# Kernel optimization log

Hardware: AMD Instinct MI355X
Metric: run time of the kernel (lower is better)

The kernel has to match this reference:

```python
import jax, jax.numpy as jnp
import numpy as np

B, C, H, W = 16, 512, 64, 64
R = 8
CP = C // R  # inner channel dim C' = 64


def setup_inputs() -> dict:
    key = jax.random.key(0)
    ks = jax.random.split(key, 10)
    s_in = 1.0 / np.sqrt(C)
    s_cp = 1.0 / np.sqrt(CP)
    return {
        "x": jax.random.normal(ks[0], (B, C, H, W), dtype=jnp.float32),
        "wq": jax.random.uniform(ks[1], (CP, C), jnp.float32, -s_in, s_in),
        "bq": jax.random.uniform(ks[2], (CP,), jnp.float32, -s_in, s_in),
        "wk": jax.random.uniform(ks[3], (CP, C), jnp.float32, -s_in, s_in),
        "bk": jax.random.uniform(ks[4], (CP,), jnp.float32, -s_in, s_in),
        "wv": jax.random.uniform(ks[5], (CP, C), jnp.float32, -s_in, s_in),
        "bv": jax.random.uniform(ks[6], (CP,), jnp.float32, -s_in, s_in),
        "wo": jax.random.uniform(ks[7], (C, CP), jnp.float32, -s_cp, s_cp),
        "bo": jax.random.uniform(ks[8], (C,), jnp.float32, -s_cp, s_cp),
        # torch init is gamma=0 (output==x, zero grads to convs); use small
        # nonzero value so the reference exercises the full graph.
        "gamma": jax.random.normal(ks[9], (1,), dtype=jnp.float32) * 0.1,
    }


def reference(x, wq, bq, wk, bk, wv, bv, wo, bo, gamma):
    b, c, h, w = x.shape
    n = h * w
    xf = x.reshape(b, c, n)  # flatten spatial -> (B, C, N)
    # 1x1 convs == channel matmuls
    q = jnp.einsum("oc,bcn->bon", wq, xf) + bq[:, None]  # (B, C', N)
    k = jnp.einsum("oc,bcn->bon", wk, xf) + bk[:, None]  # (B, C', N)
    v = jnp.einsum("oc,bcn->bon", wv, xf) + bv[:, None]  # (B, C', N)
    # energy = bmm(key (B,C',N), query^T (B,N,C')) -> (B, C', C')
    energy = jnp.einsum("bin,bjn->bij", k, q)
    attention = jax.nn.softmax(energy, axis=-1)  # (B, C', C')
    out = jnp.einsum("bij,bjn->bin", attention, v)  # (B, C', N)
    out = jnp.einsum("co,bon->bcn", wo, out) + bo[:, None]  # (B, C, N)
    out = out.reshape(b, c, h, w)
    return gamma * out + x
```

## Files before the change

kernel.cpp:

```cpp
#include <hip/hip_runtime.h>
#include <hip/hip_bf16.h>


#define NN 4096
#define CIN 512
#define CPD 64

typedef short s8v __attribute__((ext_vector_type(8)));
typedef float f4v __attribute__((ext_vector_type(4)));

__device__ __forceinline__ unsigned short f2bf(float f) {
    union { float f; unsigned int u; } c; c.f = f;
    unsigned int r = c.u + 0x7FFFu + ((c.u >> 16) & 1u);
    return (unsigned short)(r >> 16);
}

__global__ __launch_bounds__(256) void k_prep(
    const float* __restrict__ x, unsigned short* __restrict__ xt, int b_base)
{
    const int nt = blockIdx.x;
    const int ct = blockIdx.y;
    const int bl = blockIdx.z;
    const int b  = b_base + bl;
    __shared__ unsigned short lds[64][68];
    const int t = threadIdx.x;

    const float* xb = x + ((size_t)b * CIN + ct * 64) * NN + nt * 64;
    #pragma unroll
    for (int i = 0; i < 4; ++i) {
        int c = i * 16 + (t >> 4);
        int n = (t & 15) * 4;
        float4 v = *(const float4*)(xb + (size_t)c * NN + n);
        lds[c][n]     = f2bf(v.x);
        lds[c][n + 1] = f2bf(v.y);
        lds[c][n + 2] = f2bf(v.z);
        lds[c][n + 3] = f2bf(v.w);
    }
    __syncthreads();
    unsigned short* xtb = xt + ((size_t)bl * NN + nt * 64) * CIN + ct * 64;
    #pragma unroll
    for (int pass = 0; pass < 2; ++pass) {
        int n  = (t >> 3) + pass * 32;
        int c8 = (t & 7) * 8;
        unsigned short tmp[8];
        #pragma unroll
        for (int j = 0; j < 8; ++j) tmp[j] = lds[c8 + j][n];
        *(uint4*)(xtb + (size_t)n * CIN + c8) = *(const uint4*)tmp;
    }
}

__global__ __launch_bounds__(256) void k_qkv(
    const unsigned short* __restrict__ xt,
    const float* __restrict__ wq, const float* __restrict__ bq,
    const float* __restrict__ wk, const float* __restrict__ bk,
    const float* __restrict__ wv, const float* __restrict__ bv,
    unsigned short* __restrict__ q, unsigned short* __restrict__ k,
    unsigned short* __restrict__ vt, int b_base)
{
    const int nb = blockIdx.x;
    const int p  = blockIdx.y;
    const int bl = blockIdx.z;
    const int b  = b_base + bl;
    const float* w    = (p == 0) ? wq : (p == 1) ? wk : wv;
    const float* bias = (p == 0) ? bq : (p == 1) ? bk : bv;

    __shared__ unsigned short wl[64 * 512];
    const int t = threadIdx.x;

    #pragma unroll
    for (int i = 0; i < 16; ++i) {
        int lin = i * 256 + t;
        int o   = lin >> 6;
        int c8  = (lin & 63) * 8;
        float4 v0 = *(const float4*)(w + (size_t)o * CIN + c8);
        float4 v1 = *(const float4*)(w + (size_t)o * CIN + c8 + 4);
        unsigned short tmp[8] = { f2bf(v0.x), f2bf(v0.y), f2bf(v0.z), f2bf(v0.w),
                                  f2bf(v1.x), f2bf(v1.y), f2bf(v1.z), f2bf(v1.w) };
        int sw = c8 ^ ((o & 7) * 8);
        *(uint4*)(wl + o * 512 + sw) = *(const uint4*)tmp;
    }
    __syncthreads();

    const int wv_  = t >> 6;
    const int L    = t & 63;
    const int quad = L >> 4;
    const int l15  = L & 15;
    const int n0   = nb * 256 + wv_ * 64;
    const unsigned short* xb = xt + (size_t)bl * NN * CIN;

    f4v acc[4][4];
    #pragma unroll
    for (int a = 0; a < 4; ++a)
        #pragma unroll
        for (int d = 0; d < 4; ++d) acc[a][d] = (f4v){0.f, 0.f, 0.f, 0.f};

    #pragma unroll
    for (int ks = 0; ks < 16; ++ks) {
        const int c = ks * 32 + quad * 8;
        s8v bfr[4];
        #pragma unroll
        for (int nt2 = 0; nt2 < 4; ++nt2)
            bfr[nt2] = *(const s8v*)(xb + (size_t)(n0 + nt2 * 16 + l15) * CIN + c);
        s8v afr[4];
        #pragma unroll
        for (int ot = 0; ot < 4; ++ot) {
            int o = ot * 16 + l15;
            afr[ot] = *(const s8v*)(wl + o * 512 + (c ^ ((o & 7) * 8)));
        }
        #pragma unroll
        for (int ot = 0; ot < 4; ++ot)
            #pragma unroll
            for (int nt2 = 0; nt2 < 4; ++nt2)
                acc[ot][nt2] = __builtin_amdgcn_mfma_f32_16x16x32_bf16(
                    afr[ot], bfr[nt2], acc[ot][nt2], 0, 0, 0);
    }

    if (p < 2) {
        unsigned short* outp = ((p == 0) ? q : k) + (size_t)b * CPD * NN;
        #pragma unroll
        for (int ot = 0; ot < 4; ++ot)
            #pragma unroll
            for (int r = 0; r < 4; ++r) {
                int o = ot * 16 + quad * 4 + r;
                float bs = bias[o];
                #pragma unroll
                for (int nt2 = 0; nt2 < 4; ++nt2) {
                    int n = n0 + nt2 * 16 + l15;
                    outp[(size_t)o * NN + n] = f2bf(acc[ot][nt2][r] + bs);
                }
            }
    } else {
        unsigned short* outp = vt + (size_t)b * NN * CPD;
        #pragma unroll
        for (int nt2 = 0; nt2 < 4; ++nt2) {
            int n = n0 + nt2 * 16 + l15;
            #pragma unroll
            for (int ot = 0; ot < 4; ++ot) {
                unsigned short tmp[4];
                #pragma unroll
                for (int r = 0; r < 4; ++r) {
                    int o = ot * 16 + quad * 4 + r;
                    tmp[r] = f2bf(acc[ot][nt2][r] + bias[o]);
                }
                *(uint2*)(outp + (size_t)n * CPD + ot * 16 + quad * 4) = *(const uint2*)tmp;
            }
        }
    }
}

__global__ __launch_bounds__(64) void k_energy(
    const unsigned short* __restrict__ q, const unsigned short* __restrict__ k,
    float* __restrict__ epart)
{
    const int s = blockIdx.x;
    const int b = blockIdx.y;
    const int L = threadIdx.x;
    const int quad = L >> 4, l15 = L & 15;
    const unsigned short* kb = k + (size_t)b * CPD * NN;
    const unsigned short* qb = q + (size_t)b * CPD * NN;

    f4v acc[4][4];
    #pragma unroll
    for (int a = 0; a < 4; ++a)
        #pragma unroll
        for (int d = 0; d < 4; ++d) acc[a][d] = (f4v){0.f, 0.f, 0.f, 0.f};

    #pragma unroll
    for (int ks = 0; ks < 2; ++ks) {
        const int n = s * 64 + ks * 32 + quad * 8;
        s8v af[4], bf_[4];
        #pragma unroll
        for (int it = 0; it < 4; ++it)
            af[it] = *(const s8v*)(kb + (size_t)(it * 16 + l15) * NN + n);
        #pragma unroll
        for (int jt = 0; jt < 4; ++jt)
            bf_[jt] = *(const s8v*)(qb + (size_t)(jt * 16 + l15) * NN + n);
        #pragma unroll
        for (int it = 0; it < 4; ++it)
            #pragma unroll
            for (int jt = 0; jt < 4; ++jt)
                acc[it][jt] = __builtin_amdgcn_mfma_f32_16x16x32_bf16(
                    af[it], bf_[jt], acc[it][jt], 0, 0, 0);
    }
    float* ep = epart + ((size_t)b * 64 + s) * 4096;
    #pragma unroll
    for (int it = 0; it < 4; ++it)
        #pragma unroll
        for (int jt = 0; jt < 4; ++jt)
            #pragma unroll
            for (int r = 0; r < 4; ++r)
                ep[(it * 16 + quad * 4 + r) * 64 + jt * 16 + l15] = acc[it][jt][r];
}

__global__ __launch_bounds__(64) void k_softmax(
    const float* __restrict__ epart, unsigned short* __restrict__ attn)
{
    const int i = blockIdx.x;
    const int b = blockIdx.y;
    const int j = threadIdx.x;
    const float* ep = epart + (size_t)b * 64 * 4096 + i * 64 + j;
    float s = 0.f;
    #pragma unroll
    for (int sp = 0; sp < 64; ++sp) s += ep[(size_t)sp * 4096];
    float m = s;
    #pragma unroll
    for (int off = 32; off; off >>= 1) m = fmaxf(m, __shfl_xor(m, off));
    float e = __expf(s - m);
    float tot = e;
    #pragma unroll
    for (int off = 32; off; off >>= 1) tot += __shfl_xor(tot, off);
    attn[(size_t)b * 4096 + i * 64 + j] = f2bf(e / tot);
}

__global__ __launch_bounds__(256) void k_attnv(
    const unsigned short* __restrict__ vt, const unsigned short* __restrict__ attn,
    unsigned short* __restrict__ avt)
{
    const int nb = blockIdx.x;
    const int b  = blockIdx.y;
    const int t  = threadIdx.x;
    const int wv_ = t >> 6, L = t & 63, quad = L >> 4, l15 = L & 15;
    const int n0 = nb * 256 + wv_ * 64;
    const unsigned short* vtb = vt + (size_t)b * NN * CPD;
    const unsigned short* ab  = attn + (size_t)b * 4096;

    f4v acc[4][4];
    #pragma unroll
    for (int a = 0; a < 4; ++a)
        #pragma unroll
        for (int d = 0; d < 4; ++d) acc[a][d] = (f4v){0.f, 0.f, 0.f, 0.f};

    #pragma unroll
    for (int ks = 0; ks < 2; ++ks) {
        const int jc = ks * 32 + quad * 8;
        s8v af[4], bf_[4];
        #pragma unroll
        for (int mt = 0; mt < 4; ++mt)
            af[mt] = *(const s8v*)(vtb + (size_t)(n0 + mt * 16 + l15) * CPD + jc);
        #pragma unroll
        for (int it = 0; it < 4; ++it)
            bf_[it] = *(const s8v*)(ab + (size_t)(it * 16 + l15) * 64 + jc);
        #pragma unroll
        for (int mt = 0; mt < 4; ++mt)
            #pragma unroll
            for (int it = 0; it < 4; ++it)
                acc[mt][it] = __builtin_amdgcn_mfma_f32_16x16x32_bf16(
                    af[mt], bf_[it], acc[mt][it], 0, 0, 0);
    }
    unsigned short* ob = avt + (size_t)b * NN * CPD;
    #pragma unroll
    for (int mt = 0; mt < 4; ++mt)
        #pragma unroll
        for (int it = 0; it < 4; ++it) {
            int i = it * 16 + l15;
            #pragma unroll
            for (int r = 0; r < 4; ++r) {
                int n = n0 + mt * 16 + quad * 4 + r;
                ob[(size_t)n * CPD + i] = f2bf(acc[mt][it][r]);
            }
        }
}

__global__ __launch_bounds__(256) void k_out(
    const unsigned short* __restrict__ avt, const float* __restrict__ wo,
    const float* __restrict__ bo, const float* __restrict__ gamma,
    const float* __restrict__ x, float* __restrict__ out)
{
    const int nb = blockIdx.x;
    const int cb = blockIdx.y;
    const int b  = blockIdx.z;
    const int c0 = cb * 64;
    __shared__ unsigned short wl[64][72];
    const int t = threadIdx.x;

    #pragma unroll
    for (int i4 = 0; i4 < 4; ++i4) {
        int row = i4 * 16 + (t >> 4);
        int col = (t & 15) * 4;
        float4 v = *(const float4*)(wo + (size_t)(c0 + row) * CPD + col);
        unsigned short tmp[4] = { f2bf(v.x), f2bf(v.y), f2bf(v.z), f2bf(v.w) };
        *(uint2*)&wl[row][col] = *(const uint2*)tmp;
    }
    __syncthreads();

    const int wv_ = t >> 6, L = t & 63, quad = L >> 4, l15 = L & 15;
    const int n0 = nb * 256 + wv_ * 64;
    const unsigned short* avb = avt + (size_t)b * NN * CPD;

    f4v acc[4][4];
    #pragma unroll
    for (int a = 0; a < 4; ++a)
        #pragma unroll
        for (int d = 0; d < 4; ++d) acc[a][d] = (f4v){0.f, 0.f, 0.f, 0.f};

    #pragma unroll
    for (int ks = 0; ks < 2; ++ks) {
        const int ic = ks * 32 + quad * 8;
        s8v af[4], bf_[4];
        #pragma unroll
        for (int ct = 0; ct < 4; ++ct)
            af[ct] = *(const s8v*)(&wl[ct * 16 + l15][ic]);
        #pragma unroll
        for (int nt = 0; nt < 4; ++nt)
            bf_[nt] = *(const s8v*)(avb + (size_t)(n0 + nt * 16 + l15) * CPD + ic);
        #pragma unroll
        for (int ct = 0; ct < 4; ++ct)
            #pragma unroll
            for (int nt = 0; nt < 4; ++nt)
                acc[ct][nt] = __builtin_amdgcn_mfma_f32_16x16x32_bf16(
                    af[ct], bf_[nt], acc[ct][nt], 0, 0, 0);
    }

    const float g = gamma[0];
    #pragma unroll
    for (int ct = 0; ct < 4; ++ct)
        #pragma unroll
        for (int r = 0; r < 4; ++r) {
            int c = c0 + ct * 16 + quad * 4 + r;
            float bs = bo[c];
            #pragma unroll
            for (int nt = 0; nt < 4; ++nt) {
                int n = n0 + nt * 16 + l15;
                size_t idx = ((size_t)b * CIN + c) * NN + n;
                out[idx] = g * (acc[ct][nt][r] + bs) + x[idx];
            }
        }
}

extern "C" void kernel_launch(void* const* d_in, const int* in_sizes, int n_in,
                              void* d_out, int out_size, void* d_ws, size_t ws_size,
                              hipStream_t stream) {
    const float* x  = (const float*)d_in[0];
    const float* wq = (const float*)d_in[1];
    const float* bq = (const float*)d_in[2];
    const float* wk = (const float*)d_in[3];
    const float* bk = (const float*)d_in[4];
    const float* wv = (const float*)d_in[5];
    const float* bv = (const float*)d_in[6];
    const float* wo = (const float*)d_in[7];
    const float* bo = (const float*)d_in[8];
    const float* gm = (const float*)d_in[9];
    float* out = (float*)d_out;

    char* wsb = (char*)d_ws;
    unsigned short* xt = (unsigned short*)wsb;
    unsigned short* q  = (unsigned short*)(wsb + 33554432);
    unsigned short* k  = (unsigned short*)(wsb + 41943040);
    unsigned short* vt = (unsigned short*)(wsb + 50331648);
    float*          epart = (float*)wsb;
    unsigned short* attn  = (unsigned short*)(wsb + 16777216);
    unsigned short* avt   = (unsigned short*)(wsb + 25165824);

    for (int chunk = 0; chunk < 2; ++chunk) {
        int b_base = chunk * 8;
        k_prep<<<dim3(64, 8, 8), 256, 0, stream>>>(x, xt, b_base);
        k_qkv<<<dim3(16, 3, 8), 256, 0, stream>>>(xt, wq, bq, wk, bk, wv, bv,
                                                  q, k, vt, b_base);
    }
    k_energy<<<dim3(64, 16), 64, 0, stream>>>(q, k, epart);
    k_softmax<<<dim3(64, 16), 64, 0, stream>>>(epart, attn);
    k_attnv<<<dim3(16, 16), 256, 0, stream>>>(vt, attn, avt);
    k_out<<<dim3(16, 8, 16), 256, 0, stream>>>(avt, wo, bo, gm, x, out);
}
```

Measured before the change: 368.9 us.

## Fuse transpose into QKV projection, reduce energy in LDS, fuse attn-V with output conv

Removes the separate x transpose/bf16 prep kernel. The QKV kernel now reads fp32 x directly, converts it in registers, and computes all three projections per block, so x is read once instead of three times. The energy kernel uses 4 waves with an LDS atomic reduction, producing 8 partials instead of 64, which shrinks the softmax reduction. The attention-V product and output 1x1 conv are fused so the intermediate stays in LDS, at the cost of uncoalesced column-wise fp32 loads of x and a 64KB LDS weight tile per block.

```diff
diff --git a/kernel.cpp b/kernel.cpp
--- a/kernel.cpp
+++ b/kernel.cpp
@@ -15,159 +15,148 @@
     return (unsigned short)(r >> 16);
 }
 
-__global__ __launch_bounds__(256) void k_prep(
-    const float* __restrict__ x, unsigned short* __restrict__ xt, int b_base)
-{
-    const int nt = blockIdx.x;
-    const int ct = blockIdx.y;
-    const int bl = blockIdx.z;
-    const int b  = b_base + bl;
-    __shared__ unsigned short lds[64][68];
-    const int t = threadIdx.x;
-
-    const float* xb = x + ((size_t)b * CIN + ct * 64) * NN + nt * 64;
-    #pragma unroll
-    for (int i = 0; i < 4; ++i) {
-        int c = i * 16 + (t >> 4);
-        int n = (t & 15) * 4;
-        float4 v = *(const float4*)(xb + (size_t)c * NN + n);
-        lds[c][n]     = f2bf(v.x);
-        lds[c][n + 1] = f2bf(v.y);
-        lds[c][n + 2] = f2bf(v.z);
-        lds[c][n + 3] = f2bf(v.w);
-    }
-    __syncthreads();
-    unsigned short* xtb = xt + ((size_t)bl * NN + nt * 64) * CIN + ct * 64;
-    #pragma unroll
-    for (int pass = 0; pass < 2; ++pass) {
-        int n  = (t >> 3) + pass * 32;
-        int c8 = (t & 7) * 8;
-        unsigned short tmp[8];
-        #pragma unroll
-        for (int j = 0; j < 8; ++j) tmp[j] = lds[c8 + j][n];
-        *(uint4*)(xtb + (size_t)n * CIN + c8) = *(const uint4*)tmp;
-    }
-}
-
-__global__ __launch_bounds__(256) void k_qkv(
-    const unsigned short* __restrict__ xt,
+__global__ __launch_bounds__(512, 2) void k_qkv(
+    const float* __restrict__ x,
     const float* __restrict__ wq, const float* __restrict__ bq,
     const float* __restrict__ wk, const float* __restrict__ bk,
     const float* __restrict__ wv, const float* __restrict__ bv,
     unsigned short* __restrict__ q, unsigned short* __restrict__ k,
-    unsigned short* __restrict__ vt, int b_base)
+    unsigned short* __restrict__ vt)
 {
-    const int nb = blockIdx.x;
-    const int p  = blockIdx.y;
-    const int bl = blockIdx.z;
-    const int b  = b_base + bl;
-    const float* w    = (p == 0) ? wq : (p == 1) ? wk : wv;
-    const float* bias = (p == 0) ? bq : (p == 1) ? bk : bv;
-
-    __shared__ unsigned short wl[64 * 512];
+    const int nb = blockIdx.x, b = blockIdx.y;
     const int t = threadIdx.x;
-
-    #pragma unroll
-    for (int i = 0; i < 16; ++i) {
-        int lin = i * 256 + t;
-        int o   = lin >> 6;
-        int c8  = (lin & 63) * 8;
-        float4 v0 = *(const float4*)(w + (size_t)o * CIN + c8);
-        float4 v1 = *(const float4*)(w + (size_t)o * CIN + c8 + 4);
-        unsigned short tmp[8] = { f2bf(v0.x), f2bf(v0.y), f2bf(v0.z), f2bf(v0.w),
-                                  f2bf(v1.x), f2bf(v1.y), f2bf(v1.z), f2bf(v1.w) };
-        int sw = c8 ^ ((o & 7) * 8);
-        *(uint4*)(wl + o * 512 + sw) = *(const uint4*)tmp;
-    }
-    __syncthreads();
-
-    const int wv_  = t >> 6;
-    const int L    = t & 63;
-    const int quad = L >> 4;
-    const int l15  = L & 15;
-    const int n0   = nb * 256 + wv_ * 64;
-    const unsigned short* xb = xt + (size_t)bl * NN * CIN;
-
-    f4v acc[4][4];
-    #pragma unroll
-    for (int a = 0; a < 4; ++a)
-        #pragma unroll
-        for (int d = 0; d < 4; ++d) acc[a][d] = (f4v){0.f, 0.f, 0.f, 0.f};
-
-    #pragma unroll
-    for (int ks = 0; ks < 16; ++ks) {
-        const int c = ks * 32 + quad * 8;
-        s8v bfr[4];
-        #pragma unroll
-        for (int nt2 = 0; nt2 < 4; ++nt2)
-            bfr[nt2] = *(const s8v*)(xb + (size_t)(n0 + nt2 * 16 + l15) * CIN + c);
-        s8v afr[4];
+    const int wv_ = t >> 6, L = t & 63, quad = L >> 4, l15 = L & 15;
+    const int swz = (l15 & 7) * 8;
+
+    __shared__ unsigned short wl[3][64 * 128];
+
+    const float* wptr[3] = { wq, wk, wv };
+
+    f4v acc[3][4][2];
+    #pragma unroll
+    for (int p = 0; p < 3; ++p)
+        #pragma unroll
+        for (int ot = 0; ot < 4; ++ot)
+            #pragma unroll
+            for (int nn = 0; nn < 2; ++nn) acc[p][ot][nn] = (f4v){0.f,0.f,0.f,0.f};
+
+    const int n_col0 = nb * 256 + wv_ * 32 + l15;
+    const size_t xbase = (size_t)b * CIN * NN;
+
+    for (int cc = 0; cc < 4; ++cc) {
+        __syncthreads();
+        {
+            const int o   = t & 63;
+            const int c16 = (t >> 6) * 16;
+            const int osw = (o & 7) * 8;
+            #pragma unroll
+            for (int p = 0; p < 3; ++p) {
+                const float* wp = wptr[p] + (size_t)o * CIN + cc * 128 + c16;
+                unsigned short tmp[16];
+                #pragma unroll
+                for (int f = 0; f < 4; ++f) {
+                    float4 v = *(const float4*)(wp + f * 4);
+                    tmp[f*4+0] = f2bf(v.x); tmp[f*4+1] = f2bf(v.y);
+                    tmp[f*4+2] = f2bf(v.z); tmp[f*4+3] = f2bf(v.w);
+                }
+                #pragma unroll
+                for (int u = 0; u < 2; ++u)
+                    *(uint4*)&wl[p][o * 128 + ((c16 + u * 8) ^ osw)] =
+                        *(const uint4*)&tmp[u * 8];
+            }
+        }
+        __syncthreads();
+
+        #pragma unroll
+        for (int ksl = 0; ksl < 4; ++ksl) {
+            const int c = cc * 128 + ksl * 32 + quad * 8;
+            float bx0[8], bx1[8];
+            #pragma unroll
+            for (int j = 0; j < 8; ++j) {
+                const float* xc = x + xbase + (size_t)(c + j) * NN + n_col0;
+                bx0[j] = xc[0];
+                bx1[j] = xc[16];
+            }
+            s8v bf0, bf1;
+            #pragma unroll
+            for (int j = 0; j < 8; ++j) {
+                bf0[j] = (short)f2bf(bx0[j]);
+                bf1[j] = (short)f2bf(bx1[j]);
+            }
+            const int cfrag = (ksl * 32 + quad * 8) ^ swz;
+            #pragma unroll
+            for (int p = 0; p < 3; ++p)
+                #pragma unroll
+                for (int ot = 0; ot < 4; ++ot) {
+                    s8v af = *(const s8v*)&wl[p][(ot * 16 + l15) * 128 + cfrag];
+                    acc[p][ot][0] = __builtin_amdgcn_mfma_f32_16x16x32_bf16(
+                        af, bf0, acc[p][ot][0], 0, 0, 0);
+                    acc[p][ot][1] = __builtin_amdgcn_mfma_f32_16x16x32_bf16(
+                        af, bf1, acc[p][ot][1], 0, 0, 0);
+                }
+        }
+    }
+
+    const float* biasp[3] = { bq, bk, bv };
+    #pragma unroll
+    for (int p = 0; p < 2; ++p) {
+        unsigned short* outp = ((p == 0) ? q : k) + (size_t)b * CPD * NN;
         #pragma unroll
         for (int ot = 0; ot < 4; ++ot) {
-            int o = ot * 16 + l15;
-            afr[ot] = *(const s8v*)(wl + o * 512 + (c ^ ((o & 7) * 8)));
-        }
-        #pragma unroll
-        for (int ot = 0; ot < 4; ++ot)
-            #pragma unroll
-            for (int nt2 = 0; nt2 < 4; ++nt2)
-                acc[ot][nt2] = __builtin_amdgcn_mfma_f32_16x16x32_bf16(
-                    afr[ot], bfr[nt2], acc[ot][nt2], 0, 0, 0);
-    }
-
-    if (p < 2) {
-        unsigned short* outp = ((p == 0) ? q : k) + (size_t)b * CPD * NN;
-        #pragma unroll
-        for (int ot = 0; ot < 4; ++ot)
-            #pragma unroll
-            for (int r = 0; r < 4; ++r) {
-                int o = ot * 16 + quad * 4 + r;
-                float bs = bias[o];
-                #pragma unroll
-                for (int nt2 = 0; nt2 < 4; ++nt2) {
-                    int n = n0 + nt2 * 16 + l15;
-                    outp[(size_t)o * NN + n] = f2bf(acc[ot][nt2][r] + bs);
-                }
-            }
-    } else {
-        unsigned short* outp = vt + (size_t)b * NN * CPD;
-        #pragma unroll
-        for (int nt2 = 0; nt2 < 4; ++nt2) {
-            int n = n0 + nt2 * 16 + l15;
-            #pragma unroll
-            for (int ot = 0; ot < 4; ++ot) {
-                unsigned short tmp[4];
+            float4 b4 = *(const float4*)(biasp[p] + ot * 16 + quad * 4);
+            const float bsv[4] = { b4.x, b4.y, b4.z, b4.w };
+            #pragma unroll
+            for (int nn = 0; nn < 2; ++nn) {
+                const int n = n_col0 + nn * 16;
                 #pragma unroll
                 for (int r = 0; r < 4; ++r) {
                     int o = ot * 16 + quad * 4 + r;
-                    tmp[r] = f2bf(acc[ot][nt2][r] + bias[o]);
+                    outp[(size_t)o * NN + n] = f2bf(acc[p][ot][nn][r] + bsv[r]);
                 }
-                *(uint2*)(outp + (size_t)n * CPD + ot * 16 + quad * 4) = *(const uint2*)tmp;
-            }
-        }
-    }
-}
-
-__global__ __launch_bounds__(64) void k_energy(
+            }
+        }
+    }
+    {
+        unsigned short* vtb = vt + (size_t)b * NN * CPD;
+        #pragma unroll
+        for (int ot = 0; ot < 4; ++ot) {
+            float4 b4 = *(const float4*)(bv + ot * 16 + quad * 4);
+            const float bsv[4] = { b4.x, b4.y, b4.z, b4.w };
+            #pragma unroll
+            for (int nn = 0; nn < 2; ++nn) {
+                const int n = n_col0 + nn * 16;
+                unsigned short tmp[4];
+                #pragma unroll
+                for (int r = 0; r < 4; ++r) tmp[r] = f2bf(acc[2][ot][nn][r] + bsv[r]);
+                *(uint2*)(vtb + (size_t)n * CPD + ot * 16 + quad * 4) = *(const uint2*)tmp;
+            }
+        }
+    }
+}
+
+__global__ __launch_bounds__(256) void k_energy(
     const unsigned short* __restrict__ q, const unsigned short* __restrict__ k,
     float* __restrict__ epart)
 {
     const int s = blockIdx.x;
     const int b = blockIdx.y;
-    const int L = threadIdx.x;
-    const int quad = L >> 4, l15 = L & 15;
+    const int t = threadIdx.x;
+    const int wv_ = t >> 6, L = t & 63, quad = L >> 4, l15 = L & 15;
     const unsigned short* kb = k + (size_t)b * CPD * NN;
     const unsigned short* qb = q + (size_t)b * CPD * NN;
 
+    __shared__ float red[64 * 65];
+
     f4v acc[4][4];
     #pragma unroll
     for (int a = 0; a < 4; ++a)
         #pragma unroll
-        for (int d = 0; d < 4; ++d) acc[a][d] = (f4v){0.f, 0.f, 0.f, 0.f};
-
-    #pragma unroll
-    for (int ks = 0; ks < 2; ++ks) {
-        const int n = s * 64 + ks * 32 + quad * 8;
+        for (int d = 0; d < 4; ++d) acc[a][d] = (f4v){0.f,0.f,0.f,0.f};
+
+    const int nbase = s * 512 + wv_ * 128;
+    #pragma unroll
+    for (int ks = 0; ks < 4; ++ks) {
+        const int n = nbase + ks * 32 + quad * 8;
         s8v af[4], bf_[4];
         #pragma unroll
         for (int it = 0; it < 4; ++it)
@@ -182,14 +171,21 @@
                 acc[it][jt] = __builtin_amdgcn_mfma_f32_16x16x32_bf16(
                     af[it], bf_[jt], acc[it][jt], 0, 0, 0);
     }
-    float* ep = epart + ((size_t)b * 64 + s) * 4096;
+
+    for (int idx = t; idx < 64 * 65; idx += 256) red[idx] = 0.f;
+    __syncthreads();
     #pragma unroll
     for (int it = 0; it < 4; ++it)
         #pragma unroll
         for (int jt = 0; jt < 4; ++jt)
             #pragma unroll
             for (int r = 0; r < 4; ++r)
-                ep[(it * 16 + quad * 4 + r) * 64 + jt * 16 + l15] = acc[it][jt][r];
+                atomicAdd(&red[(it * 16 + quad * 4 + r) * 65 + jt * 16 + l15],
+                          acc[it][jt][r]);
+    __syncthreads();
+    float* ep = epart + ((size_t)b * 8 + s) * 4096;
+    for (int idx = t; idx < 4096; idx += 256)
+        ep[idx] = red[(idx >> 6) * 65 + (idx & 63)];
 }
 
 __global__ __launch_bounds__(64) void k_softmax(
@@ -198,10 +194,10 @@
     const int i = blockIdx.x;
     const int b = blockIdx.y;
     const int j = threadIdx.x;
-    const float* ep = epart + (size_t)b * 64 * 4096 + i * 64 + j;
     float s = 0.f;
     #pragma unroll
-    for (int sp = 0; sp < 64; ++sp) s += ep[(size_t)sp * 4096];
+    for (int sp = 0; sp < 8; ++sp)
+        s += epart[((size_t)b * 8 + sp) * 4096 + i * 64 + j];
     float m = s;
     #pragma unroll
     for (int off = 32; off; off >>= 1) m = fmaxf(m, __shfl_xor(m, off));
@@ -212,119 +208,123 @@
     attn[(size_t)b * 4096 + i * 64 + j] = f2bf(e / tot);
 }
 
-__global__ __launch_bounds__(256) void k_attnv(
+__global__ __launch_bounds__(256) void k_avout(
     const unsigned short* __restrict__ vt, const unsigned short* __restrict__ attn,
-    unsigned short* __restrict__ avt)
+    const float* __restrict__ wo, const float* __restrict__ bo,
+    const float* __restrict__ gamma, const float* __restrict__ x,
+    float* __restrict__ out)
 {
-    const int nb = blockIdx.x;
-    const int b  = blockIdx.y;
-    const int t  = threadIdx.x;
+    const int nb = blockIdx.x, b = blockIdx.y;
+    const int t = threadIdx.x;
     const int wv_ = t >> 6, L = t & 63, quad = L >> 4, l15 = L & 15;
-    const int n0 = nb * 256 + wv_ * 64;
-    const unsigned short* vtb = vt + (size_t)b * NN * CPD;
-    const unsigned short* ab  = attn + (size_t)b * 4096;
-
-    f4v acc[4][4];
-    #pragma unroll
-    for (int a = 0; a < 4; ++a)
-        #pragma unroll
-        for (int d = 0; d < 4; ++d) acc[a][d] = (f4v){0.f, 0.f, 0.f, 0.f};
-
-    #pragma unroll
-    for (int ks = 0; ks < 2; ++ks) {
-        const int jc = ks * 32 + quad * 8;
-        s8v af[4], bf_[4];
-        #pragma unroll
-        for (int mt = 0; mt < 4; ++mt)
-            af[mt] = *(const s8v*)(vtb + (size_t)(n0 + mt * 16 + l15) * CPD + jc);
+    const int swz = (l15 & 7) * 8;
+
+    __shared__ unsigned short wol[512 * 64];
+    __shared__ unsigned short avl[128 * 64];
+
+    {
+        const int i16 = (t & 3) * 16;
+        #pragma unroll
+        for (int pass = 0; pass < 8; ++pass) {
+            const int c = (t >> 2) + pass * 64;
+            const int csw = (c & 7) * 8;
+            const float* wp = wo + (size_t)c * CPD + i16;
+            unsigned short tmp[16];
+            #pragma unroll
+            for (int f = 0; f < 4; ++f) {
+                float4 v = *(const float4*)(wp + f * 4);
+                tmp[f*4+0] = f2bf(v.x); tmp[f*4+1] = f2bf(v.y);
+                tmp[f*4+2] = f2bf(v.z); tmp[f*4+3] = f2bf(v.w);
+            }
+            #pragma unroll
+            for (int u = 0; u < 2; ++u)
+                *(uint4*)&wol[c * 64 + ((i16 + u * 8) ^ csw)] = *(const uint4*)&tmp[u*8];
+        }
+    }
+
+    {
+        const unsigned short* ab  = attn + (size_t)b * 4096;
+        const unsigned short* vtb = vt + (size_t)b * NN * CPD;
+        const int n0 = nb * 128;
+        f4v acc1[4][2];
+        #pragma unroll
+        for (int a = 0; a < 4; ++a)
+            #pragma unroll
+            for (int d = 0; d < 2; ++d) acc1[a][d] = (f4v){0.f,0.f,0.f,0.f};
+        #pragma unroll
+        for (int ks = 0; ks < 2; ++ks) {
+            const int j = ks * 32 + quad * 8;
+            s8v af[4], bf_[2];
+            #pragma unroll
+            for (int it = 0; it < 4; ++it)
+                af[it] = *(const s8v*)(ab + (size_t)(it * 16 + l15) * 64 + j);
+            #pragma unroll
+            for (int nn = 0; nn < 2; ++nn)
+                bf_[nn] = *(const s8v*)(vtb +
+                    (size_t)(n0 + wv_ * 32 + nn * 16 + l15) * CPD + j);
+            #pragma unroll
+            for (int it = 0; it < 4; ++it)
+                #pragma unroll
+                for (int nn = 0; nn < 2; ++nn)
+                    acc1[it][nn] = __builtin_amdgcn_mfma_f32_16x16x32_bf16(
+                        af[it], bf_[nn], acc1[it][nn], 0, 0, 0);
+        }
         #pragma unroll
         for (int it = 0; it < 4; ++it)
-            bf_[it] = *(const s8v*)(ab + (size_t)(it * 16 + l15) * 64 + jc);
-        #pragma unroll
-        for (int mt = 0; mt < 4; ++mt)
-            #pragma unroll
-            for (int it = 0; it < 4; ++it)
-                acc[mt][it] = __builtin_amdgcn_mfma_f32_16x16x32_bf16(
-                    af[mt], bf_[it], acc[mt][it], 0, 0, 0);
-    }
-    unsigned short* ob = avt + (size_t)b * NN * CPD;
-    #pragma unroll
-    for (int mt = 0; mt < 4; ++mt)
-        #pragma unroll
-        for (int it = 0; it < 4; ++it) {
-            int i = it * 16 + l15;
-            #pragma unroll
-            for (int r = 0; r < 4; ++r) {
-                int n = n0 + mt * 16 + quad * 4 + r;
-                ob[(size_t)n * CPD + i] = f2bf(acc[mt][it][r]);
-            }
-        }
-}
-
-__global__ __launch_bounds__(256) void k_out(
-    const unsigned short* __restrict__ avt, const float* __restrict__ wo,
-    const float* __restrict__ bo, const float* __restrict__ gamma,
-    const float* __restrict__ x, float* __restrict__ out)
-{
-    const int nb = blockIdx.x;
-    const int cb = blockIdx.y;
-    const int b  = blockIdx.z;
-    const int c0 = cb * 64;
-    __shared__ unsigned short wl[64][72];
-    const int t = threadIdx.x;
-
-    #pragma unroll
-    for (int i4 = 0; i4 < 4; ++i4) {
-        int row = i4 * 16 + (t >> 4);
-        int col = (t & 15) * 4;
-        float4 v = *(const float4*)(wo + (size_t)(c0 + row) * CPD + col);
-        unsigned short tmp[4] = { f2bf(v.x), f2bf(v.y), f2bf(v.z), f2bf(v.w) };
-        *(uint2*)&wl[row][col] = *(const uint2*)tmp;
+            #pragma unroll
+            for (int nn = 0; nn < 2; ++nn) {
+                const int nloc = wv_ * 32 + nn * 16 + l15;
+                unsigned short tmp[4];
+                #pragma unroll
+                for (int r = 0; r < 4; ++r) tmp[r] = f2bf(acc1[it][nn][r]);
+                *(uint2*)&avl[nloc * 64 + ((it * 16 + quad * 4) ^ swz)] =
+                    *(const uint2*)tmp;
+            }
     }
     __syncthreads();
 
-    const int wv_ = t >> 6, L = t & 63, quad = L >> 4, l15 = L & 15;
-    const int n0 = nb * 256 + wv_ * 64;
-    const unsigned short* avb = avt + (size_t)b * NN * CPD;
-
-    f4v acc[4][4];
-    #pragma unroll
-    for (int a = 0; a < 4; ++a)
-        #pragma unroll
-        for (int d = 0; d < 4; ++d) acc[a][d] = (f4v){0.f, 0.f, 0.f, 0.f};
-
-    #pragma unroll
-    for (int ks = 0; ks < 2; ++ks) {
-        const int ic = ks * 32 + quad * 8;
-        s8v af[4], bf_[4];
-        #pragma unroll
-        for (int ct = 0; ct < 4; ++ct)
-            af[ct] = *(const s8v*)(&wl[ct * 16 + l15][ic]);
-        #pragma unroll
-        for (int nt = 0; nt < 4; ++nt)
-            bf_[nt] = *(const s8v*)(avb + (size_t)(n0 + nt * 16 + l15) * CPD + ic);
-        #pragma unroll
-        for (int ct = 0; ct < 4; ++ct)
-            #pragma unroll
-            for (int nt = 0; nt < 4; ++nt)
-                acc[ct][nt] = __builtin_amdgcn_mfma_f32_16x16x32_bf16(
-                    af[ct], bf_[nt], acc[ct][nt], 0, 0, 0);
-    }
-
     const float g = gamma[0];
-    #pragma unroll
-    for (int ct = 0; ct < 4; ++ct)
-        #pragma unroll
-        for (int r = 0; r < 4; ++r) {
-            int c = c0 + ct * 16 + quad * 4 + r;
-            float bs = bo[c];
-            #pragma unroll
-            for (int nt = 0; nt < 4; ++nt) {
-                int n = n0 + nt * 16 + l15;
-                size_t idx = ((size_t)b * CIN + c) * NN + n;
-                out[idx] = g * (acc[ct][nt][r] + bs) + x[idx];
-            }
-        }
+    const int n0 = nb * 128;
+    for (int cb = 0; cb < 8; ++cb) {
+        f4v acc2[2][4];
+        #pragma unroll
+        for (int a = 0; a < 2; ++a)
+            #pragma unroll
+            for (int d = 0; d < 4; ++d) acc2[a][d] = (f4v){0.f,0.f,0.f,0.f};
+        #pragma unroll
+        for (int ks = 0; ks < 2; ++ks) {
+            const int ic = (ks * 32 + quad * 8) ^ swz;
+            s8v af2[2], bf2[4];
+            #pragma unroll
+            for (int nt = 0; nt < 2; ++nt)
+                af2[nt] = *(const s8v*)&avl[(wv_ * 32 + nt * 16 + l15) * 64 + ic];
+            #pragma unroll
+            for (int ct = 0; ct < 4; ++ct)
+                bf2[ct] = *(const s8v*)&wol[(cb * 64 + ct * 16 + l15) * 64 + ic];
+            #pragma unroll
+            for (int nt = 0; nt < 2; ++nt)
+                #pragma unroll
+                for (int ct = 0; ct < 4; ++ct)
+                    acc2[nt][ct] = __builtin_amdgcn_mfma_f32_16x16x32_bf16(
+                        af2[nt], bf2[ct], acc2[nt][ct], 0, 0, 0);
+        }
+        #pragma unroll
+        for (int nt = 0; nt < 2; ++nt)
+            #pragma unroll
+            for (int ct = 0; ct < 4; ++ct) {
+                const int c = cb * 64 + ct * 16 + l15;
+                const float bs = bo[c];
+                const int nbase = n0 + wv_ * 32 + nt * 16 + quad * 4;
+                const size_t idx = ((size_t)b * CIN + c) * NN + nbase;
+                float4 xr = *(const float4*)(x + idx);
+                float4 r4;
+                r4.x = g * (acc2[nt][ct][0] + bs) + xr.x;
+                r4.y = g * (acc2[nt][ct][1] + bs) + xr.y;
+                r4.z = g * (acc2[nt][ct][2] + bs) + xr.z;
+                r4.w = g * (acc2[nt][ct][3] + bs) + xr.w;
+                *(float4*)(out + idx) = r4;
+            }
+    }
 }
 
 extern "C" void kernel_launch(void* const* d_in, const int* in_sizes, int n_in,
@@ -343,22 +343,14 @@
     float* out = (float*)d_out;
 
     char* wsb = (char*)d_ws;
-    unsigned short* xt = (unsigned short*)wsb;
-    unsigned short* q  = (unsigned short*)(wsb + 33554432);
-    unsigned short* k  = (unsigned short*)(wsb + 41943040);
-    unsigned short* vt = (unsigned short*)(wsb + 50331648);
-    float*          epart = (float*)wsb;
-    unsigned short* attn  = (unsigned short*)(wsb + 16777216);
-    unsigned short* avt   = (unsigned short*)(wsb + 25165824);
-
-    for (int chunk = 0; chunk < 2; ++chunk) {
-        int b_base = chunk * 8;
-        k_prep<<<dim3(64, 8, 8), 256, 0, stream>>>(x, xt, b_base);
-        k_qkv<<<dim3(16, 3, 8), 256, 0, stream>>>(xt, wq, bq, wk, bk, wv, bv,
-                                                  q, k, vt, b_base);
-    }
-    k_energy<<<dim3(64, 16), 64, 0, stream>>>(q, k, epart);
+    unsigned short* q     = (unsigned short*)wsb;
+    unsigned short* k     = (unsigned short*)(wsb + 8388608);
+    unsigned short* vt    = (unsigned short*)(wsb + 16777216);
+    float*          epart = (float*)(wsb + 25165824);
+    unsigned short* attn  = (unsigned short*)(wsb + 27262976);
+
+    k_qkv<<<dim3(16, 16), 512, 0, stream>>>(x, wq, bq, wk, bk, wv, bv, q, k, vt);
+    k_energy<<<dim3(8, 16), 256, 0, stream>>>(q, k, epart);
     k_softmax<<<dim3(64, 16), 64, 0, stream>>>(epart, attn);
-    k_attnv<<<dim3(16, 16), 256, 0, stream>>>(vt, attn, avt);
-    k_out<<<dim3(16, 8, 16), 256, 0, stream>>>(avt, wo, bo, gm, x, out);
-}
+    k_avout<<<dim3(32, 16), 256, 0, stream>>>(vt, attn, wo, bo, gm, x, out);
+}
```

After: 339.7 us. 1.09x faster.
